# Kernel optimization log

Measured on AMD Instinct MI355X. Metric: run time of the kernel, lower is better.

Reference implementation:

```python
import jax, jax.numpy as jnp
import numpy as np

B, N_IN, N_HID, N_OUT = 1024, 1024, 2048, 32000


def setup_inputs() -> dict:
    key = jax.random.key(0)
    ks = jax.random.split(key, 9)
    s = lambda fan_in: 1.0 / np.sqrt(fan_in)
    return {
        "input": jax.random.normal(ks[0], (B, N_IN), jnp.float32),
        "hidden": jax.random.normal(ks[1], (B, N_HID), jnp.float32),
        "W_i2g": jax.random.normal(ks[2], (2 * N_HID, N_IN + N_HID), jnp.float32) * s(N_IN + N_HID),
        "b_i2g": jax.random.normal(ks[3], (2 * N_HID,), jnp.float32) * s(N_IN + N_HID),
        "W_x2h": jax.random.normal(ks[4], (N_HID, N_IN), jnp.float32) * s(N_IN),
        "b_x2h": jax.random.normal(ks[5], (N_HID,), jnp.float32) * s(N_IN),
        "W_h2h": jax.random.normal(ks[6], (N_HID, N_HID), jnp.float32) * s(N_HID),
        "W_h2o": jax.random.normal(ks[7], (N_OUT, N_HID), jnp.float32) * s(N_HID),
        "b_h2o": jax.random.normal(ks[8], (N_OUT,), jnp.float32) * s(N_HID),
    }


def reference(input, hidden, W_i2g, b_i2g, W_x2h, b_x2h, W_h2h, W_h2o, b_h2o):
    # combined = cat([input, hidden], dim=1); gates = sigmoid(i2g(combined))
    combined = jnp.concatenate([input, hidden], axis=1)           # [B, n_in+n_hid]
    gates = jax.nn.sigmoid(combined @ W_i2g.T + b_i2g)            # [B, 2*n_hid]
    z, r = gates[:, :N_HID], gates[:, N_HID:]
    # candidate h: tanh(x2h(x) + h2h(r*h)); GRU blend
    h_cand = jnp.tanh(input @ W_x2h.T + b_x2h + (r * hidden) @ W_h2h.T)
    h = z * hidden + (1.0 - z) * h_cand                           # [B, n_hid]
    # dropout in eval mode = identity; h2o + log_softmax over dim 1
    logits = h @ W_h2o.T + b_h2o                                  # [B, n_out]
    output = jax.nn.log_softmax(logits, axis=1)
    return (output, h)
```

## Files before the change

kernel.cpp:

```cpp
#include <hip/hip_runtime.h>
#include <hip/hip_bf16.h>
#include <stdint.h>

using bf16 = __hip_bfloat16;
typedef __bf16 bf16x8 __attribute__((ext_vector_type(8)));
typedef float f32x4 __attribute__((ext_vector_type(4)));

__device__ __forceinline__ void gload_lds16(const bf16* g, bf16* l) {
  __builtin_amdgcn_global_load_lds(
      (const __attribute__((address_space(1))) void*)g,
      (__attribute__((address_space(3))) void*)l, 16, 0, 0);
}

#define BARRIER() asm volatile("s_barrier" ::: "memory")

struct CvtArgs {
  const float* src[5];
  bf16* dst[5];
  int n[5];
  int bstart[6];
};

__global__ __launch_bounds__(256) void cvt_all(CvtArgs a) {
  int seg = 0;
#pragma unroll
  for (int i = 0; i < 4; ++i)
    if ((int)blockIdx.x >= a.bstart[i + 1]) seg = i + 1;
  const int nb = a.bstart[seg + 1] - a.bstart[seg];
  const int lb = blockIdx.x - a.bstart[seg];
  const float* __restrict__ in = a.src[seg];
  bf16* __restrict__ out = a.dst[seg];
  const int n = a.n[seg];
  const int stride = nb * 256 * 4;
  for (int i = (lb * 256 + (int)threadIdx.x) * 4; i < n; i += stride) {
    float4 v = *reinterpret_cast<const float4*>(in + i);
    union { bf16 h[4]; uint2 u; } o;
    o.h[0] = __float2bfloat16(v.x);
    o.h[1] = __float2bfloat16(v.y);
    o.h[2] = __float2bfloat16(v.z);
    o.h[3] = __float2bfloat16(v.w);
    *reinterpret_cast<uint2*>(out + i) = o.u;
  }
}

template <int EPI>
__global__ __launch_bounds__(256)
void gemm128(const bf16* __restrict__ A0, const bf16* __restrict__ A1,
             int aSplit, int ldA0, int ldA1,
             const bf16* __restrict__ B0, const bf16* __restrict__ B1,
             int bSplit, int ldB0, int ldB1,
             int MB, int N, int K,
             const float* __restrict__ bias,
             const float* __restrict__ hidden,
             const bf16* __restrict__ zbuf,
             bf16* __restrict__ obf_a,
             bf16* __restrict__ obf_b,
             float* __restrict__ of32,
             int gemmBlocks,
             const float* __restrict__ csrc,
             bf16* __restrict__ cdst, int cn) {
  const int tid = threadIdx.x;
  if ((int)blockIdx.x >= gemmBlocks) {
    const int cb = blockIdx.x - gemmBlocks;
    const int ncb = gridDim.x - gemmBlocks;
    const int stride = ncb * 256 * 4;
    for (int i = (cb * 256 + tid) * 4; i < cn; i += stride) {
      float4 v = *reinterpret_cast<const float4*>(csrc + i);
      union { bf16 h[4]; uint2 u; } o;
      o.h[0] = __float2bfloat16(v.x);
      o.h[1] = __float2bfloat16(v.y);
      o.h[2] = __float2bfloat16(v.z);
      o.h[3] = __float2bfloat16(v.w);
      *reinterpret_cast<uint2*>(cdst + i) = o.u;
    }
    return;
  }
  __shared__ bf16 lA[128 * 32];
  __shared__ bf16 lB[128 * 32];
  const int wave = tid >> 6;
  const int lane = tid & 63;
  const int cpx = gemmBlocks >> 3;
  const int swz = ((int)blockIdx.x & 7) * cpx + ((int)blockIdx.x >> 3);
  const int bm = swz % MB;
  const int bn = swz / MB;
  const int wr = wave >> 1, wc = wave & 1;
  const int l4 = lane >> 2;
  const int lk8 = (lane & 3) * 8;
  const int lrow = lane & 15;
  const int lk = (lane >> 4) * 8;

  f32x4 acc[4][4] = {};

  const int nkt = K >> 5;
  for (int kt = 0; kt < nkt; ++kt) {
    const int kb = kt << 5;
    {
      const bf16* Ap; int lda, klocA;
      if (kb < aSplit) { Ap = A0; lda = ldA0; klocA = kb; }
      else             { Ap = A1; lda = ldA1; klocA = kb - aSplit; }
      const bf16* Bp; int ldb, klocB;
      if (kb < bSplit) { Bp = B0; ldb = ldB0; klocB = kb; }
      else             { Bp = B1; ldb = ldB1; klocB = kb - bSplit; }
#pragma unroll
      for (int r = 0; r < 2; ++r) {
        const int rowb = (r * 4 + wave) * 16;
        gload_lds16(Ap + (size_t)(bm * 128 + rowb + l4) * lda + klocA + lk8,
                    &lA[rowb * 32]);
        gload_lds16(Bp + (size_t)(bn * 128 + rowb + l4) * ldb + klocB + lk8,
                    &lB[rowb * 32]);
      }
    }
    __syncthreads();
    bf16x8 af[4], bfr[4];
#pragma unroll
    for (int f = 0; f < 4; ++f)
      af[f] = *reinterpret_cast<const bf16x8*>(
          &lA[(wr * 64 + f * 16 + lrow) * 32 + lk]);
#pragma unroll
    for (int f = 0; f < 4; ++f)
      bfr[f] = *reinterpret_cast<const bf16x8*>(
          &lB[(wc * 64 + f * 16 + lrow) * 32 + lk]);
#pragma unroll
    for (int fm = 0; fm < 4; ++fm)
#pragma unroll
      for (int fn = 0; fn < 4; ++fn)
        acc[fm][fn] = __builtin_amdgcn_mfma_f32_16x16x32_bf16(
            af[fm], bfr[fn], acc[fm][fn], 0, 0, 0);
    __syncthreads();
  }

  const int rb = bm * 128 + wr * 64 + (lane >> 4) * 4;
  const int cb = bn * 128 + wc * 64 + lrow;
#pragma unroll
  for (int fm = 0; fm < 4; ++fm) {
#pragma unroll
    for (int fn = 0; fn < 4; ++fn) {
#pragma unroll
      for (int j = 0; j < 4; ++j) {
        const int m = rb + fm * 16 + j;
        const int n = cb + fn * 16;
        float v = acc[fm][fn][j];
        if (EPI == 1) {
          v = 1.0f / (1.0f + __expf(-(v + bias[n])));
          if (n < 2048) {
            obf_a[(size_t)m * 2048 + n] = __float2bfloat16(v);
          } else {
            const int nn = n - 2048;
            obf_b[(size_t)m * 2048 + nn] =
                __float2bfloat16(v * hidden[(size_t)m * 2048 + nn]);
          }
        } else if (EPI == 2) {
          const float e = __expf(2.0f * (v + bias[n]));
          const float hc = (e - 1.0f) / (e + 1.0f);
          const float z = __bfloat162float(zbuf[(size_t)m * 2048 + n]);
          const float hd = hidden[(size_t)m * 2048 + n];
          const float h = z * hd + (1.0f - z) * hc;
          of32[(size_t)m * 2048 + n] = h;
          obf_a[(size_t)m * 2048 + n] = __float2bfloat16(h);
        }
      }
    }
  }
}

__global__ __launch_bounds__(512, 2)
void gemm256_f(const bf16* __restrict__ A, const bf16* __restrict__ W,
               const float* __restrict__ bias, uint32_t* __restrict__ lgt,
               float2* __restrict__ partials, int MB, int K, int NPB) {
  __shared__ bf16 lds[5][256 * 64];
  const int tid = threadIdx.x;
  const int w = tid >> 6, lane = tid & 63;
  const int nwg = gridDim.x;
  const int q8 = nwg >> 3, r8 = nwg & 7;
  const int xcd = (int)blockIdx.x & 7, lid = (int)blockIdx.x >> 3;
  const int swz =
      (xcd < r8 ? xcd * (q8 + 1) : r8 * (q8 + 1) + (xcd - r8) * q8) + lid;
  const int bm = swz % MB, bn = swz / MB;
  const int wr = w >> 2, wc = w & 3;
  const int l8 = lane >> 3;
  const int gcol = ((lane & 7) ^ l8) * 8;
  const int rA = lane & 15;
  const int kb0 = (lane >> 4) * 16;
  const int xm = (lane & 7) << 4;
  const int nkt = K >> 6, niter = nkt >> 1;
  const bf16* gA = A + (size_t)bm * 256 * K;
  const bf16* gB = W + (size_t)bn * 256 * K;

  auto STAGE2 = [&](int plane, int kt, const bf16* g) {
    if (kt > nkt - 1) kt = nkt - 1;
#pragma unroll
    for (int h = 0; h < 2; ++h) {
      const int r0 = h * 128 + w * 16;
#pragma unroll
      for (int j = 0; j < 2; ++j)
        gload_lds16(g + (size_t)(r0 + j * 8 + l8) * K + kt * 64 + gcol,
                    &lds[plane][(r0 + j * 8) * 64]);
    }
  };
  auto RD = [&](int plane, int row, int ks) {
    const int off = row * 128 + ((ks * 64 + kb0) ^ xm);
    return *reinterpret_cast<const bf16x8*>(
        reinterpret_cast<const char*>(&lds[plane][0]) + off);
  };

  f32x4 acc[8][4] = {};

  int a0 = 0, a1 = 1, a2 = 2;
  STAGE2(a0, 0, gA); STAGE2(3, 0, gB);
  STAGE2(a1, 1, gA); STAGE2(4, 1, gB);
  asm volatile("s_waitcnt vmcnt(8)" ::: "memory");
  BARRIER();

  for (int it = 0; it < niter; ++it) {
    const int t = it << 1;
    const bool last = (it == niter - 1);
    bf16x8 bfr[4][2];
#pragma unroll
    for (int ph = 0; ph < 8; ++ph) {
      const int buf = ph >> 2, q = ph & 3;
      const int ap = buf ? a1 : a0;
      const int bp = 3 + buf;
      bf16x8 af[2][2];
      if (q == 0) {
#pragma unroll
        for (int n = 0; n < 4; ++n)
#pragma unroll
          for (int ks = 0; ks < 2; ++ks)
            bfr[n][ks] = RD(bp, wc * 64 + n * 16 + rA, ks);
      }
#pragma unroll
      for (int mm = 0; mm < 2; ++mm)
#pragma unroll
        for (int ks = 0; ks < 2; ++ks)
          af[mm][ks] = RD(ap, wr * 128 + (q * 2 + mm) * 16 + rA, ks);

      if (ph == 0)      STAGE2(a2, t + 2, gA);
      else if (ph == 1) STAGE2(3, t + 2, gB);
      else if (ph == 4) STAGE2(a0, t + 3, gA);
      else if (ph == 5) STAGE2(4, t + 3, gB);

      __builtin_amdgcn_s_setprio(1);
#pragma unroll
      for (int mm = 0; mm < 2; ++mm)
#pragma unroll
        for (int n = 0; n < 4; ++n)
#pragma unroll
          for (int ks = 0; ks < 2; ++ks)
            acc[q * 2 + mm][n] = __builtin_amdgcn_mfma_f32_16x16x32_bf16(
                af[mm][ks], bfr[n][ks], acc[q * 2 + mm][n], 0, 0, 0);
      __builtin_amdgcn_s_setprio(0);

      if (ph == 3 || ph == 7)
        asm volatile("s_waitcnt vmcnt(8)" ::: "memory");
      if (!(ph == 7 && last)) BARRIER();
    }
    const int na0 = a2, na1 = a0, na2 = a1;
    a0 = na0; a1 = na1; a2 = na2;
  }
  asm volatile("s_waitcnt vmcnt(0) lgkmcnt(0)" ::: "memory");
  __syncthreads();

  float* red = (float*)&lds[0][0];
  float* red2 = red + 1024;
  const int outc = bn * 256 + wc * 64 + rA;
  float bb[4];
#pragma unroll
  for (int n = 0; n < 4; ++n) bb[n] = bias[outc + n * 16];
#pragma unroll
  for (int m = 0; m < 8; ++m)
#pragma unroll
    for (int n = 0; n < 4; ++n)
#pragma unroll
      for (int j = 0; j < 4; ++j) acc[m][n][j] += bb[n];

  const int q4 = lane >> 4;
  const int rowb = wr * 128 + q4 * 4;
#pragma unroll
  for (int m = 0; m < 8; ++m)
#pragma unroll
    for (int j = 0; j < 4; ++j) {
      float x = fmaxf(fmaxf(acc[m][0][j], acc[m][1][j]),
                      fmaxf(acc[m][2][j], acc[m][3][j]));
      x = fmaxf(x, __shfl_xor(x, 1));
      x = fmaxf(x, __shfl_xor(x, 2));
      x = fmaxf(x, __shfl_xor(x, 4));
      x = fmaxf(x, __shfl_xor(x, 8));
      if (rA == 0) red[wc * 256 + rowb + m * 16 + j] = x;
    }
  __syncthreads();
  if (tid < 256)
    red2[tid] = fmaxf(fmaxf(red[0 * 256 + tid], red[1 * 256 + tid]),
                      fmaxf(red[2 * 256 + tid], red[3 * 256 + tid]));
  __syncthreads();

  uint32_t* lgtb = lgt + (size_t)(bm * NPB + bn) * (64 * 512) + tid;
#pragma unroll
  for (int m = 0; m < 8; ++m) {
    const int r0 = rowb + m * 16;
    float s[4];
#pragma unroll
    for (int j = 0; j < 4; ++j) {
      const float fm = red2[r0 + j];
      float e = __expf(acc[m][0][j] - fm) + __expf(acc[m][1][j] - fm) +
                __expf(acc[m][2][j] - fm) + __expf(acc[m][3][j] - fm);
      e += __shfl_xor(e, 1);
      e += __shfl_xor(e, 2);
      e += __shfl_xor(e, 4);
      e += __shfl_xor(e, 8);
      s[j] = e;
    }
#pragma unroll
    for (int j = 0; j < 4; ++j)
      if (rA == 0) red[wc * 256 + r0 + j] = s[j];
#pragma unroll
    for (int n = 0; n < 4; ++n)
#pragma unroll
      for (int k = 0; k < 2; ++k) {
        union { bf16 h[2]; uint32_t u; } pk;
        pk.h[0] = __float2bfloat16(acc[m][n][2 * k]);
        pk.h[1] = __float2bfloat16(acc[m][n][2 * k + 1]);
        lgtb[(size_t)(m * 8 + n * 2 + k) * 512] = pk.u;
      }
  }
  __syncthreads();
  if (tid < 256) {
    const float ssum = red[0 * 256 + tid] + red[1 * 256 + tid] +
                       red[2 * 256 + tid] + red[3 * 256 + tid];
    partials[(size_t)(bm * 256 + tid) * NPB + bn] =
        make_float2(red2[tid], ssum);
  }
}

__global__ __launch_bounds__(128) void lse_reduce(
    const float2* __restrict__ partials, float* __restrict__ lse, int NPB) {
  const int row = blockIdx.x;
  const int t = threadIdx.x;
  float m = -3.4e38f, s = 0.0f;
  if (t < NPB) {
    float2 p = partials[(size_t)row * NPB + t];
    m = p.x;
    s = p.y;
  }
#pragma unroll
  for (int o = 32; o; o >>= 1) {
    const float om = __shfl_xor(m, o), os = __shfl_xor(s, o);
    const float nm = fmaxf(m, om);
    s = s * __expf(m - nm) + os * __expf(om - nm);
    m = nm;
  }
  __shared__ float sm[2], ss[2];
  if ((t & 63) == 0) { sm[t >> 6] = m; ss[t >> 6] = s; }
  __syncthreads();
  if (t == 0) {
    const float M = fmaxf(sm[0], sm[1]);
    const float S = ss[0] * __expf(sm[0] - M) + ss[1] * __expf(sm[1] - M);
    lse[row] = M + __logf(S);
  }
}

__global__ __launch_bounds__(512) void ls_final(
    const uint32_t* __restrict__ lgt, const float* __restrict__ lse,
    float* __restrict__ out, int NPB) {
  const int blk = blockIdx.x;
  const int bm = blk / NPB, bn = blk % NPB;
  const int t = threadIdx.x;
  const int w = t >> 6, lane = t & 63;
  const int wr = w >> 2, wc = w & 3, q4 = lane >> 4, rAc = lane & 15;
  const uint32_t* src = lgt + (size_t)blk * (64 * 512) + t;
  const int col = bn * 256 + wc * 64 + rAc;
  const int row0 = bm * 256 + wr * 128 + q4 * 4;
#pragma unroll 4
  for (int fp = 0; fp < 64; ++fp) {
    const int m = fp >> 3, n = (fp >> 1) & 3, k = fp & 1;
    const uint32_t u = src[(size_t)fp * 512];
    const int r = row0 + m * 16 + 2 * k;
    const int c = col + n * 16;
    const float lo = __uint_as_float(u << 16);
    const float hi = __uint_as_float(u & 0xffff0000u);
    out[(size_t)r * 32000 + c] = lo - lse[r];
    out[(size_t)(r + 1) * 32000 + c] = hi - lse[r + 1];
  }
}

extern "C" void kernel_launch(void* const* d_in, const int* in_sizes, int n_in,
                              void* d_out, int out_size, void* d_ws,
                              size_t ws_size, hipStream_t stream) {
  const float* input  = (const float*)d_in[0];
  const float* hidden = (const float*)d_in[1];
  const float* W_i2g  = (const float*)d_in[2];
  const float* b_i2g  = (const float*)d_in[3];
  const float* W_x2h  = (const float*)d_in[4];
  const float* b_x2h  = (const float*)d_in[5];
  const float* W_h2h  = (const float*)d_in[6];
  const float* W_h2o  = (const float*)d_in[7];
  const float* b_h2o  = (const float*)d_in[8];

  float* out_ls = (float*)d_out;
  float* out_h  = out_ls + (size_t)1024 * 32000;

  char* ws = (char*)d_ws;
  bf16* inp_bf     = (bf16*)(ws + 0);
  bf16* hid_bf     = (bf16*)(ws + 2097152);
  bf16* wi_bf      = (bf16*)(ws + 6291456);
  bf16* wx_bf      = (bf16*)(ws + 31457280);
  bf16* wh_bf      = (bf16*)(ws + 35651584);
  bf16* z_bf       = (bf16*)(ws + 44040192);
  bf16* rh_bf      = (bf16*)(ws + 48234496);
  bf16* h_bf       = (bf16*)(ws + 52428800);
  bf16* wo_bf      = (bf16*)(ws + 56623104);
  uint32_t* lgt    = (uint32_t*)(ws + 187695104);
  float2* partials = (float2*)(ws + 253231104);
  float* lse       = (float*)(ws + 254255104);

  CvtArgs ca;
  ca.src[0] = input;  ca.dst[0] = inp_bf; ca.n[0] = 1024 * 1024;
  ca.src[1] = hidden; ca.dst[1] = hid_bf; ca.n[1] = 1024 * 2048;
  ca.src[2] = W_i2g;  ca.dst[2] = wi_bf;  ca.n[2] = 4096 * 3072;
  ca.src[3] = W_x2h;  ca.dst[3] = wx_bf;  ca.n[3] = 2048 * 1024;
  ca.src[4] = W_h2h;  ca.dst[4] = wh_bf;  ca.n[4] = 2048 * 2048;
  const int bs[6] = {0, 24, 72, 370, 418, 512};
  for (int i = 0; i < 6; ++i) ca.bstart[i] = bs[i];
  cvt_all<<<512, 256, 0, stream>>>(ca);

  const int HALF_WO = 32000 * 2048 / 2;

  gemm128<1><<<256 + 256, 256, 0, stream>>>(
      inp_bf, hid_bf, 1024, 1024, 2048,
      wi_bf, wi_bf, 1 << 30, 3072, 3072,
      8, 4096, 3072, b_i2g, hidden, nullptr, z_bf, rh_bf, nullptr,
      256, W_h2o, wo_bf, HALF_WO);

  gemm128<2><<<128 + 384, 256, 0, stream>>>(
      inp_bf, rh_bf, 1024, 1024, 2048,
      wx_bf, wh_bf, 1024, 1024, 2048,
      8, 2048, 3072, b_x2h, hidden, z_bf, h_bf, nullptr, out_h,
      128, W_h2o + HALF_WO, wo_bf + HALF_WO, HALF_WO);

  gemm256_f<<<4 * 125, 512, 0, stream>>>(h_bf, wo_bf, b_h2o, lgt, partials,
                                         4, 2048, 125);

  lse_reduce<<<1024, 128, 0, stream>>>(partials, lse, 125);
  ls_final<<<500, 512, 0, stream>>>(lgt, lse, out_ls, 125);
}
```

Measured before the change: 433.6 us.

## Double-buffer LDS with BK=64 and XOR-swizzled layout in GEMM mainloop

Moves the GEMM mainloop from a single-buffered K=32 tile to a double-buffered K=64 tile, issuing the next tile's global-to-LDS loads before computing on the current one. It also XOR-swizzles the LDS layout to avoid bank conflicts on fragment reads and raises wave priority around the MFMA block. The aim is to hide global load latency and halve the number of barriers per K. In exchange LDS use rises to 64KB per block, which can reduce occupancy.

```diff
diff --git a/kernel.cpp b/kernel.cpp
--- a/kernel.cpp
+++ b/kernel.cpp
@@ -75,8 +75,8 @@
     }
     return;
   }
-  __shared__ bf16 lA[128 * 32];
-  __shared__ bf16 lB[128 * 32];
+  __shared__ bf16 lA[2][128 * 64];
+  __shared__ bf16 lB[2][128 * 64];
   const int wave = tid >> 6;
   const int lane = tid & 63;
   const int cpx = gemmBlocks >> 3;
@@ -84,49 +84,73 @@
   const int bm = swz % MB;
   const int bn = swz / MB;
   const int wr = wave >> 1, wc = wave & 1;
-  const int l4 = lane >> 2;
-  const int lk8 = (lane & 3) * 8;
+  const int l8 = lane >> 3;
+  const int gcol = ((lane & 7) ^ l8) * 8;
   const int lrow = lane & 15;
-  const int lk = (lane >> 4) * 8;
+  const int kb0 = (lane >> 4) * 16;
+  const int xm = (lane & 7) << 4;
+  const int nkt = K >> 6;
+
+  auto STAGEK = [&](int buf, int kt) {
+    if (kt >= nkt) return;
+    const int kb = kt << 6;
+    const bf16* Ap; int lda, ka;
+    if (kb < aSplit) { Ap = A0; lda = ldA0; ka = kb; }
+    else             { Ap = A1; lda = ldA1; ka = kb - aSplit; }
+    const bf16* Bp; int ldb, kbb;
+    if (kb < bSplit) { Bp = B0; ldb = ldB0; kbb = kb; }
+    else             { Bp = B1; ldb = ldB1; kbb = kb - bSplit; }
+#pragma unroll
+    for (int h = 0; h < 2; ++h)
+#pragma unroll
+      for (int j = 0; j < 2; ++j) {
+        const int r0 = h * 64 + wave * 16 + j * 8;
+        gload_lds16(Ap + (size_t)(bm * 128 + r0 + l8) * lda + ka + gcol,
+                    &lA[buf][r0 * 64]);
+        gload_lds16(Bp + (size_t)(bn * 128 + r0 + l8) * ldb + kbb + gcol,
+                    &lB[buf][r0 * 64]);
+      }
+  };
+  auto RDA = [&](int buf, int row, int ks) {
+    return *reinterpret_cast<const bf16x8*>(
+        reinterpret_cast<const char*>(&lA[buf][0]) + row * 128 +
+        ((ks * 64 + kb0) ^ xm));
+  };
+  auto RDB = [&](int buf, int row, int ks) {
+    return *reinterpret_cast<const bf16x8*>(
+        reinterpret_cast<const char*>(&lB[buf][0]) + row * 128 +
+        ((ks * 64 + kb0) ^ xm));
+  };
 
   f32x4 acc[4][4] = {};
 
-  const int nkt = K >> 5;
+  STAGEK(0, 0);
+  asm volatile("s_waitcnt vmcnt(0)" ::: "memory");
+  BARRIER();
+
   for (int kt = 0; kt < nkt; ++kt) {
-    const int kb = kt << 5;
-    {
-      const bf16* Ap; int lda, klocA;
-      if (kb < aSplit) { Ap = A0; lda = ldA0; klocA = kb; }
-      else             { Ap = A1; lda = ldA1; klocA = kb - aSplit; }
-      const bf16* Bp; int ldb, klocB;
-      if (kb < bSplit) { Bp = B0; ldb = ldB0; klocB = kb; }
-      else             { Bp = B1; ldb = ldB1; klocB = kb - bSplit; }
-#pragma unroll
-      for (int r = 0; r < 2; ++r) {
-        const int rowb = (r * 4 + wave) * 16;
-        gload_lds16(Ap + (size_t)(bm * 128 + rowb + l4) * lda + klocA + lk8,
-                    &lA[rowb * 32]);
-        gload_lds16(Bp + (size_t)(bn * 128 + rowb + l4) * ldb + klocB + lk8,
-                    &lB[rowb * 32]);
+    const int buf = kt & 1;
+    STAGEK(buf ^ 1, kt + 1);
+    bf16x8 af[4][2], bfr[4][2];
+#pragma unroll
+    for (int f = 0; f < 4; ++f)
+#pragma unroll
+      for (int ks = 0; ks < 2; ++ks) {
+        af[f][ks] = RDA(buf, wr * 64 + f * 16 + lrow, ks);
+        bfr[f][ks] = RDB(buf, wc * 64 + f * 16 + lrow, ks);
       }
-    }
-    __syncthreads();
-    bf16x8 af[4], bfr[4];
-#pragma unroll
-    for (int f = 0; f < 4; ++f)
-      af[f] = *reinterpret_cast<const bf16x8*>(
-          &lA[(wr * 64 + f * 16 + lrow) * 32 + lk]);
-#pragma unroll
-    for (int f = 0; f < 4; ++f)
-      bfr[f] = *reinterpret_cast<const bf16x8*>(
-          &lB[(wc * 64 + f * 16 + lrow) * 32 + lk]);
+    __builtin_amdgcn_s_setprio(1);
 #pragma unroll
     for (int fm = 0; fm < 4; ++fm)
 #pragma unroll
       for (int fn = 0; fn < 4; ++fn)
-        acc[fm][fn] = __builtin_amdgcn_mfma_f32_16x16x32_bf16(
-            af[fm], bfr[fn], acc[fm][fn], 0, 0, 0);
-    __syncthreads();
+#pragma unroll
+        for (int ks = 0; ks < 2; ++ks)
+          acc[fm][fn] = __builtin_amdgcn_mfma_f32_16x16x32_bf16(
+              af[fm][ks], bfr[fn][ks], acc[fm][fn], 0, 0, 0);
+    __builtin_amdgcn_s_setprio(0);
+    asm volatile("s_waitcnt vmcnt(0)" ::: "memory");
+    BARRIER();
   }
 
   const int rb = bm * 128 + wr * 64 + (lane >> 4) * 4;
```

Result: faster. 369.1 us, median of 2 (-14.9%).
